# Performance work log

Measured on AMD Instinct MI355X. Metric: run time of the kernel, lower is better.

The kernel has to match this reference:

```python
import jax, jax.numpy as jnp
import numpy as np

WS = 8          # window_size
HEADS = 6
DH = 32         # dim_head


def _dwconv(t, w):
    # t: (B,C,H,W), w: (C,1,3,3) depthwise, stride 1, padding 1 -> SAME
    return jax.lax.conv_general_dilated(
        t, w, window_strides=(1, 1), padding='SAME',
        feature_group_count=t.shape[1],
        dimension_numbers=('NCHW', 'OIHW', 'NCHW'))


def _l2norm(t, eps=1e-12):
    # matches F.normalize: x / max(||x||, eps)
    n = jnp.sqrt(jnp.sum(t * t, axis=-1, keepdims=True))
    return t / jnp.maximum(n, eps)


def setup_inputs() -> dict:
    key = jax.random.key(0)
    ks = jax.random.split(key, 10)
    B, H, W, C = 2, 256, 256, 192
    s = 0.05
    return {
        'x': jax.random.normal(ks[0], (B, H, W, C), jnp.float32),
        'illu_fea_trans': jax.random.normal(ks[1], (B, H, W, C), jnp.float32),
        'gt_w': jax.random.normal(ks[2], (C, C), jnp.float32) * s,
        'gt_b': jax.random.normal(ks[3], (C,), jnp.float32) * s,
        'qkv_w': jax.random.normal(ks[4], (C, 3 * C), jnp.float32) * s,
        'qkv_b': jax.random.normal(ks[5], (3 * C,), jnp.float32) * s,
        'proj_w': jax.random.normal(ks[6], (C, C), jnp.float32) * s,
        'proj_b': jax.random.normal(ks[7], (C,), jnp.float32) * s,
        'conv1_w': jax.random.normal(ks[8], (C, 1, 3, 3), jnp.float32) * s,
        'conv2_w': jax.random.normal(ks[9], (C, 1, 3, 3), jnp.float32) * s,
    }


def reference(x, illu_fea_trans, gt_w, gt_b, qkv_w, qkv_b, proj_w, proj_b,
              conv1_w, conv2_w):
    B, H, W, C = x.shape
    Ws, heads, d = WS, HEADS, DH
    scale = d ** (-0.5)
    pad_h = (Ws - H % Ws) % Ws
    pad_w = (Ws - W % Ws) % Ws
    xp = jnp.pad(x, ((0, 0), (0, pad_h), (0, pad_w), (0, 0)), mode='reflect')
    ip = jnp.pad(illu_fea_trans, ((0, 0), (0, pad_h), (0, pad_w), (0, 0)), mode='reflect')
    Hp, Wp = xp.shape[1], xp.shape[2]
    nW = (Hp // Ws) * (Wp // Ws)
    T = Ws * Ws

    def to_windows(t):
        t = t.reshape(B, Hp // Ws, Ws, Wp // Ws, Ws, C)
        return t.transpose(0, 1, 3, 2, 4, 5).reshape(B * nW, T, C)

    xw = to_windows(xp)                                  # (B*nW, T, C)
    qkv = (xw @ qkv_w + qkv_b).reshape(B * nW, T, 3, heads, d)
    qkv = qkv.transpose(2, 0, 3, 1, 4)                   # (3, Bn, h, T, d)
    q, k, v = qkv[0], qkv[1], qkv[2]
    q = _l2norm(q)
    k = _l2norm(k)

    illu = to_windows(ip).reshape(B * nW, T, heads, d).transpose(0, 2, 1, 3)
    v = v * (1.0 + jax.nn.sigmoid(illu))

    # global token: avg-pool over padded spatial dims, then linear
    gt = jnp.mean(xp, axis=(1, 2)) @ gt_w + gt_b          # (B, C)
    gt = gt.reshape(B, heads, 1, d)
    # faithful to torch expand(dim=2 -> nW).reshape(B*nW, heads, 1, d)
    gk = jnp.broadcast_to(gt, (B, heads, nW, d)).reshape(B * nW, heads, 1, d)
    k = jnp.concatenate([k, gk], axis=2)                  # (Bn, h, T+1, d)
    v = jnp.concatenate([v, gk], axis=2)

    # chunked softmax over keys == full softmax over key axis (chunks on q only)
    attn = jax.nn.softmax(jnp.einsum('bhqd,bhkd->bhqk', q, k) * scale, axis=-1)
    out = jnp.einsum('bhqk,bhkd->bhqd', attn, v)          # (Bn, h, T, d)
    out = out.transpose(0, 2, 1, 3).reshape(B * nW, T, C)
    out = out @ proj_w + proj_b

    out = out.reshape(B, Hp // Ws, Wp // Ws, Ws, Ws, C)
    out = out.transpose(0, 1, 3, 2, 4, 5).reshape(B, Hp, Wp, C)[:, :H, :W, :]

    # depthwise-conv positional branch on padded x (exact gelu like torch)
    t = xp.transpose(0, 3, 1, 2)                          # (B,C,Hp,Wp)
    t = _dwconv(t, conv1_w)
    t = jax.nn.gelu(t, approximate=False)
    t = _dwconv(t, conv2_w)
    pos = t.transpose(0, 2, 3, 1)[:, :H, :W, :]
    return out + pos
```

## Files before the change

kernel.cpp:

```cpp
#include <hip/hip_runtime.h>
#include <hip/hip_bf16.h>

#define BB   2
#define HH   256
#define WWD  256
#define CC   192
#define WSZ  8
#define TT   64
#define NHD  6
#define DHD  32
#define N3   576

typedef __attribute__((ext_vector_type(8))) short short8;
typedef __attribute__((ext_vector_type(4))) float f32x4;

__device__ inline short bf16_bits(float f) {
  __hip_bfloat16 h = __float2bfloat16(f);
  return __builtin_bit_cast(short, h);
}

__device__ inline void stage1k(const short* gsrc, short* ldst, int lane) {
  __builtin_amdgcn_global_load_lds(
      (const __attribute__((address_space(1))) void*)(gsrc + lane * 8),
      (__attribute__((address_space(3))) void*)ldst, 16, 0, 0);
}

__global__ __launch_bounds__(256) void lcam_wshuf(const float* __restrict__ src,
                                                  short* __restrict__ dst,
                                                  int ncols, int nfrag, int perm) {
  int gid = blockIdx.x * 256 + threadIdx.x;
  if (gid >= nfrag) return;
  int lane = gid & 63;
  int s = (gid >> 6) % 6;
  int ct = gid / 384;
  int col = ct * 16 + (lane & 15);
  int k0 = s * 32 + (lane >> 4) * 8;
  short8 v;
#pragma unroll
  for (int j = 0; j < 8; ++j)
    v[j] = bf16_bits(src[(size_t)(k0 + j) * ncols + col]);
  int didx = perm ? ((s * (ncols / 16) + ct) * 64 + lane) : gid;
  *(short8*)(dst + (size_t)didx * 8) = v;
}

__global__ __launch_bounds__(256) void lcam_sum_x(const float* __restrict__ x,
                                                  float* __restrict__ sums) {
  int blk = blockIdx.x;
  int b = blk >> 9;
  int chunk = blk & 511;
  const float* xp = x + ((size_t)b * 65536 + (size_t)chunk * 128) * CC;
  int t = threadIdx.x;
  if (t < CC) {
    float acc = 0.f;
    for (int p = 0; p < 128; ++p) acc += xp[(size_t)p * CC + t];
    atomicAdd(&sums[b * CC + t], acc);
  }
}

__global__ void lcam_gt(const float* __restrict__ sums,
                        const float* __restrict__ gt_w,
                        const float* __restrict__ gt_b,
                        float* __restrict__ gt) {
  int b = blockIdx.x;
  int co = threadIdx.x;
  float acc = gt_b[co];
  const float inv = 1.f / 65536.f;
  for (int c = 0; c < CC; ++c)
    acc += sums[b * CC + c] * inv * gt_w[c * CC + co];
  gt[b * CC + co] = acc;
}

__global__ __launch_bounds__(256) void lcam_attn(
    const float* __restrict__ x, const float* __restrict__ illu,
    const short* __restrict__ wf, const short* __restrict__ pwf,
    const float* __restrict__ qkv_b, const float* __restrict__ proj_b,
    const float* __restrict__ gt, float* __restrict__ out) {
  __shared__ __align__(16) short wgt[2][6144];
  __shared__ __align__(16) short ks[65 * 40];
  __shared__ __align__(16) short vt[32 * 72];
  __shared__ __align__(16) short qs[64 * 40];
  __shared__ __align__(16) short ps[64 * 72];

  int w = blockIdx.x;
  int b  = w >> 10;
  int wy = (w >> 5) & 31;
  int wx = w & 31;
  int t  = threadIdx.x;
  int lane = t & 63;
  int rtile = t >> 6;
  int m = lane & 15;
  int quad = lane >> 4;
  int key0 = rtile * 16 + quad * 4;

  size_t base = ((size_t)(b * HH + wy * WSZ) * WWD + wx * WSZ) * CC;

#pragma unroll
  for (int u = 0; u < 3; ++u) {
    int ii = rtile * 3 + u;
    stage1k(wf + ii * 512, wgt[0] + ii * 512, lane);
  }

  int apix = rtile * 16 + m;
  size_t arow = base + (size_t)((apix >> 3) * WWD + (apix & 7)) * CC + quad * 8;
  short8 afrag[6];
#pragma unroll
  for (int s = 0; s < 6; ++s) {
    const float* ap = x + arow + s * 32;
    float4 f0 = *(const float4*)(ap);
    float4 f1 = *(const float4*)(ap + 4);
    short8 v;
    v[0] = bf16_bits(f0.x); v[1] = bf16_bits(f0.y);
    v[2] = bf16_bits(f0.z); v[3] = bf16_bits(f0.w);
    v[4] = bf16_bits(f1.x); v[5] = bf16_bits(f1.y);
    v[6] = bf16_bits(f1.z); v[7] = bf16_bits(f1.w);
    afrag[s] = v;
  }
  const short8* wA8 = (const short8*)wgt[0];
  const short8* wB8 = (const short8*)wgt[1];

  f32x4 pacc[12];
#pragma unroll
  for (int ct = 0; ct < 12; ++ct) {
    f32x4 z = {0.f, 0.f, 0.f, 0.f};
    pacc[ct] = z;
  }

  __syncthreads();

  for (int h = 0; h < NHD; ++h) {
#pragma unroll
    for (int u = 0; u < 3; ++u) {
      int ii = rtile * 3 + u;
      stage1k(wf + (12 + 2 * h) * 3072 + ii * 512, wgt[1] + ii * 512, lane);
    }
    float gv0 = gt[b * CC + h * 32 + m];
    float gv1 = gt[b * CC + h * 32 + 16 + m];
    float il0[4], il1[4];
#pragma unroll
    for (int r = 0; r < 4; ++r) {
      int key = key0 + r;
      const float* ip = illu + base + (size_t)((key >> 3) * WWD + (key & 7)) * CC + h * 32;
      il0[r] = ip[m];
      il1[r] = ip[16 + m];
    }
    {
      f32x4 a0 = {0.f,0.f,0.f,0.f}, a1 = {0.f,0.f,0.f,0.f};
      __builtin_amdgcn_s_setprio(1);
#pragma unroll
      for (int s = 0; s < 6; ++s)
        a0 = __builtin_amdgcn_mfma_f32_16x16x32_bf16(afrag[s], wA8[s*64 + lane], a0, 0,0,0);
#pragma unroll
      for (int s = 0; s < 6; ++s)
        a1 = __builtin_amdgcn_mfma_f32_16x16x32_bf16(afrag[s], wA8[384 + s*64 + lane], a1, 0,0,0);
      __builtin_amdgcn_s_setprio(0);
      float b0 = qkv_b[h*32 + m], b1 = qkv_b[h*32 + 16 + m];
#pragma unroll
      for (int r = 0; r < 4; ++r) {
        float v0 = a0[r] + b0, v1 = a1[r] + b1;
        float ss = v0*v0 + v1*v1;
        ss += __shfl_xor(ss, 1); ss += __shfl_xor(ss, 2);
        ss += __shfl_xor(ss, 4); ss += __shfl_xor(ss, 8);
        float scl = 0.17677669529663688f * __builtin_amdgcn_rsqf(fmaxf(ss, 1e-24f));
        int row = key0 + r;
        qs[row*40 + m]      = bf16_bits(v0 * scl);
        qs[row*40 + 16 + m] = bf16_bits(v1 * scl);
      }
    }
    __syncthreads();
#pragma unroll
    for (int u = 0; u < 3; ++u) {
      int ii = rtile * 3 + u;
      stage1k(wf + (24 + 2 * h) * 3072 + ii * 512, wgt[0] + ii * 512, lane);
    }
    {
      f32x4 a0 = {0.f,0.f,0.f,0.f}, a1 = {0.f,0.f,0.f,0.f};
      __builtin_amdgcn_s_setprio(1);
#pragma unroll
      for (int s = 0; s < 6; ++s)
        a0 = __builtin_amdgcn_mfma_f32_16x16x32_bf16(afrag[s], wB8[s*64 + lane], a0, 0,0,0);
#pragma unroll
      for (int s = 0; s < 6; ++s)
        a1 = __builtin_amdgcn_mfma_f32_16x16x32_bf16(afrag[s], wB8[384 + s*64 + lane], a1, 0,0,0);
      __builtin_amdgcn_s_setprio(0);
      float b0 = qkv_b[192 + h*32 + m], b1 = qkv_b[192 + h*32 + 16 + m];
#pragma unroll
      for (int r = 0; r < 4; ++r) {
        float v0 = a0[r] + b0, v1 = a1[r] + b1;
        float ss = v0*v0 + v1*v1;
        ss += __shfl_xor(ss, 1); ss += __shfl_xor(ss, 2);
        ss += __shfl_xor(ss, 4); ss += __shfl_xor(ss, 8);
        float scl = __builtin_amdgcn_rsqf(fmaxf(ss, 1e-24f));
        int row = key0 + r;
        ks[row*40 + m]      = bf16_bits(v0 * scl);
        ks[row*40 + 16 + m] = bf16_bits(v1 * scl);
      }
    }
    __syncthreads();
#pragma unroll
    for (int u = 0; u < 3; ++u) {
      int ii = rtile * 3 + u;
      stage1k(pwf + h * 6144 + ii * 512, wgt[1] + ii * 512, lane);
    }
    {
      f32x4 a0 = {0.f,0.f,0.f,0.f}, a1 = {0.f,0.f,0.f,0.f};
      __builtin_amdgcn_s_setprio(1);
#pragma unroll
      for (int s = 0; s < 6; ++s)
        a0 = __builtin_amdgcn_mfma_f32_16x16x32_bf16(afrag[s], wA8[s*64 + lane], a0, 0,0,0);
#pragma unroll
      for (int s = 0; s < 6; ++s)
        a1 = __builtin_amdgcn_mfma_f32_16x16x32_bf16(afrag[s], wA8[384 + s*64 + lane], a1, 0,0,0);
      __builtin_amdgcn_s_setprio(0);
      float b0 = qkv_b[384 + h*32 + m], b1 = qkv_b[384 + h*32 + 16 + m];
#pragma unroll
      for (int r = 0; r < 4; ++r) {
        int key = key0 + r;
        float s0 = __builtin_amdgcn_rcpf(1.f + __expf(-il0[r]));
        float s1 = __builtin_amdgcn_rcpf(1.f + __expf(-il1[r]));
        vt[m*72 + key]        = bf16_bits((a0[r] + b0) * (1.f + s0));
        vt[(16 + m)*72 + key] = bf16_bits((a1[r] + b1) * (1.f + s1));
      }
    }
    if (t < DHD) ks[64*40 + t] = bf16_bits(gt[b*CC + h*DHD + t]);
    __syncthreads();
    if (h < NHD - 1) {
#pragma unroll
      for (int u = 0; u < 3; ++u) {
        int ii = rtile * 3 + u;
        stage1k(wf + 2 * (h + 1) * 3072 + ii * 512, wgt[0] + ii * 512, lane);
      }
    }
    short8 qa = *(const short8*)(qs + (rtile*16 + m)*40 + quad*8);
    f32x4 sc[5];
#pragma unroll
    for (int ct = 0; ct < 4; ++ct) {
      short8 kb = *(const short8*)(ks + (ct*16 + m)*40 + quad*8);
      f32x4 z = {0.f,0.f,0.f,0.f};
      sc[ct] = __builtin_amdgcn_mfma_f32_16x16x32_bf16(qa, kb, z, 0,0,0);
    }
    {
      short8 kb = *(const short8*)(ks + 64*40 + quad*8);
      f32x4 z = {0.f,0.f,0.f,0.f};
      sc[4] = __builtin_amdgcn_mfma_f32_16x16x32_bf16(qa, kb, z, 0,0,0);
    }
    float p64v[4], invr[4];
#pragma unroll
    for (int r = 0; r < 4; ++r) {
      float e0 = __expf(sc[0][r]), e1 = __expf(sc[1][r]);
      float e2 = __expf(sc[2][r]), e3 = __expf(sc[3][r]);
      float e4 = (m == 0) ? __expf(sc[4][r]) : 0.f;
      int row = key0 + r;
      ps[row*72 + m]      = bf16_bits(e0);
      ps[row*72 + 16 + m] = bf16_bits(e1);
      ps[row*72 + 32 + m] = bf16_bits(e2);
      ps[row*72 + 48 + m] = bf16_bits(e3);
      float sum = e0 + e1 + e2 + e3 + e4;
      sum += __shfl_xor(sum, 1); sum += __shfl_xor(sum, 2);
      sum += __shfl_xor(sum, 4); sum += __shfl_xor(sum, 8);
      invr[r] = __builtin_amdgcn_rcpf(sum);
      p64v[r] = e4;
    }
    f32x4 o0 = {0.f,0.f,0.f,0.f}, o1 = {0.f,0.f,0.f,0.f};
    __builtin_amdgcn_s_setprio(1);
#pragma unroll
    for (int kc = 0; kc < 2; ++kc) {
      short8 pa  = *(const short8*)(ps + (rtile*16 + m)*72 + kc*32 + quad*8);
      short8 vb0 = *(const short8*)(vt + m*72        + kc*32 + quad*8);
      short8 vb1 = *(const short8*)(vt + (16 + m)*72 + kc*32 + quad*8);
      o0 = __builtin_amdgcn_mfma_f32_16x16x32_bf16(pa, vb0, o0, 0,0,0);
      o1 = __builtin_amdgcn_mfma_f32_16x16x32_bf16(pa, vb1, o1, 0,0,0);
    }
    __builtin_amdgcn_s_setprio(0);
#pragma unroll
    for (int r = 0; r < 4; ++r) {
      float pr = __shfl(p64v[r], lane & 48);
      int row = key0 + r;
      qs[row*40 + m]      = bf16_bits((o0[r] + pr * gv0) * invr[r]);
      qs[row*40 + 16 + m] = bf16_bits((o1[r] + pr * gv1) * invr[r]);
    }
    short8 oa = *(const short8*)(qs + (rtile*16 + m)*40 + quad*8);
    __builtin_amdgcn_s_setprio(1);
#pragma unroll
    for (int ct = 0; ct < 12; ++ct)
      pacc[ct] = __builtin_amdgcn_mfma_f32_16x16x32_bf16(oa, wB8[ct*64 + lane], pacc[ct], 0,0,0);
    __builtin_amdgcn_s_setprio(0);
    __syncthreads();
  }
#pragma unroll
  for (int ct = 0; ct < 12; ++ct) {
    float bias = proj_b[ct*16 + m];
#pragma unroll
    for (int r = 0; r < 4; ++r) {
      int row = key0 + r;
      out[base + (size_t)((row >> 3) * WWD + (row & 7)) * CC + ct*16 + m] = pacc[ct][r] + bias;
    }
  }
}

__global__ __launch_bounds__(256) void lcam_pos(const float* __restrict__ x,
                                                const float* __restrict__ w1,
                                                const float* __restrict__ w2,
                                                float* __restrict__ out) {
  __shared__ __align__(16) float xt[20 * 20 * 16];
  __shared__ float t1[18 * 18 * 16];
  __shared__ float wl1[16 * 9], wl2[16 * 9];
  int blk = blockIdx.x;
  int cgI = blk % 12; int tmp = blk / 12;
  int tx = tmp % 16; tmp /= 16;
  int ty = tmp % 16; int b = tmp / 16;
  int c0 = cgI * 16;
  int y0 = ty * 16, x0 = tx * 16;
  int t = threadIdx.x;
  if (t < 144) { wl1[t] = w1[c0 * 9 + t]; wl2[t] = w2[c0 * 9 + t]; }
  for (int vi = t; vi < 1600; vi += 256) {
    int cc4 = vi & 3;
    int lin = vi >> 2;
    int xx = lin % 20, yy = lin / 20;
    int gy = y0 - 2 + yy, gx = x0 - 2 + xx;
    float4 v = {0.f, 0.f, 0.f, 0.f};
    if (gy >= 0 && gy < HH && gx >= 0 && gx < WWD)
      v = *(const float4*)(x + (((size_t)b * HH + gy) * WWD + gx) * CC + c0 + cc4 * 4);
    *(float4*)(xt + (yy * 20 + xx) * 16 + cc4 * 4) = v;
  }
  __syncthreads();
  for (int idx = t; idx < 5184; idx += 256) {
    int cc = idx & 15;
    int xx = (idx >> 4) % 18;
    int yy = idx / 288;
    int gy = y0 - 1 + yy, gx = x0 - 1 + xx;
    float r = 0.f;
    if (gy >= 0 && gy < HH && gx >= 0 && gx < WWD) {
#pragma unroll
      for (int ky = 0; ky < 3; ++ky)
#pragma unroll
        for (int kx = 0; kx < 3; ++kx)
          r += xt[((yy + ky) * 20 + xx + kx) * 16 + cc] * wl1[cc * 9 + ky * 3 + kx];
      r = 0.5f * r * (1.f + erff(r * 0.70710678118654752f));
    }
    t1[(yy * 18 + xx) * 16 + cc] = r;
  }
  __syncthreads();
  for (int idx = t; idx < 4096; idx += 256) {
    int cc = idx & 15;
    int xx = (idx >> 4) & 15;
    int yy = idx >> 8;
    float r = 0.f;
#pragma unroll
    for (int ky = 0; ky < 3; ++ky)
#pragma unroll
      for (int kx = 0; kx < 3; ++kx)
        r += t1[((yy + ky) * 18 + xx + kx) * 16 + cc] * wl2[cc * 9 + ky * 3 + kx];
    size_t o = (((size_t)b * HH + y0 + yy) * WWD + x0 + xx) * CC + c0 + cc;
    out[o] += r;
  }
}

extern "C" void kernel_launch(void* const* d_in, const int* in_sizes, int n_in,
                              void* d_out, int out_size, void* d_ws, size_t ws_size,
                              hipStream_t stream) {
  const float* x       = (const float*)d_in[0];
  const float* illu    = (const float*)d_in[1];
  const float* gt_w    = (const float*)d_in[2];
  const float* gt_b    = (const float*)d_in[3];
  const float* qkv_w   = (const float*)d_in[4];
  const float* qkv_b   = (const float*)d_in[5];
  const float* proj_w  = (const float*)d_in[6];
  const float* proj_b  = (const float*)d_in[7];
  const float* conv1_w = (const float*)d_in[8];
  const float* conv2_w = (const float*)d_in[9];
  float* out = (float*)d_out;

  short* wf   = (short*)d_ws;
  short* pwf  = (short*)((char*)d_ws + 221184);
  float* sums = (float*)((char*)d_ws + 221184 + 73728);
  float* gt   = sums + BB * CC;

  hipMemsetAsync(sums, 0, BB * CC * sizeof(float), stream);
  lcam_wshuf<<<54, 256, 0, stream>>>(qkv_w, wf, N3, 36 * 6 * 64, 0);
  lcam_wshuf<<<18, 256, 0, stream>>>(proj_w, pwf, CC, 12 * 6 * 64, 1);
  lcam_sum_x<<<1024, 256, 0, stream>>>(x, sums);
  lcam_gt<<<BB, CC, 0, stream>>>(sums, gt_w, gt_b, gt);
  lcam_attn<<<2048, 256, 0, stream>>>(x, illu, wf, pwf, qkv_b, proj_b, gt, out);
  lcam_pos<<<6144, 256, 0, stream>>>(x, conv1_w, conv2_w, out);
}
```

Before: 504.4 us.

## Vectorize depthwise conv and channel sum, merge weight shuffle launches

The positional conv kernel now has each thread handle four channels with float4 LDS reads, keeps the 3x3 weights in registers, and does a float4 read-modify-write on the output. The channel-sum kernel reads float4 across four row groups and reduces them in shared memory before the atomics. The two weight-shuffle launches are merged into one kernel. The aim is fewer LDS and global instructions, better load parallelism in the reductions, and less launch overhead, at the cost of more registers in the conv kernel.

```diff
diff --git a/kernel.cpp b/kernel.cpp
--- a/kernel.cpp
+++ b/kernel.cpp
@@ -25,35 +25,54 @@
       (__attribute__((address_space(3))) void*)ldst, 16, 0, 0);
 }
 
-__global__ __launch_bounds__(256) void lcam_wshuf(const float* __restrict__ src,
-                                                  short* __restrict__ dst,
-                                                  int ncols, int nfrag, int perm) {
+__global__ __launch_bounds__(256) void lcam_wshuf2(const float* __restrict__ qkv_w,
+                                                   const float* __restrict__ proj_w,
+                                                   short* __restrict__ wf,
+                                                   short* __restrict__ pwf) {
   int gid = blockIdx.x * 256 + threadIdx.x;
-  if (gid >= nfrag) return;
-  int lane = gid & 63;
-  int s = (gid >> 6) % 6;
-  int ct = gid / 384;
+  const float* src; short* dst; int ncols, perm, g;
+  if (gid < 13824) { src = qkv_w; dst = wf; ncols = N3; perm = 0; g = gid; }
+  else {
+    g = gid - 13824;
+    if (g >= 4608) return;
+    src = proj_w; dst = pwf; ncols = CC; perm = 1;
+  }
+  int lane = g & 63;
+  int s = (g >> 6) % 6;
+  int ct = g / 384;
   int col = ct * 16 + (lane & 15);
   int k0 = s * 32 + (lane >> 4) * 8;
   short8 v;
 #pragma unroll
   for (int j = 0; j < 8; ++j)
     v[j] = bf16_bits(src[(size_t)(k0 + j) * ncols + col]);
-  int didx = perm ? ((s * (ncols / 16) + ct) * 64 + lane) : gid;
+  int didx = perm ? ((s * (ncols / 16) + ct) * 64 + lane) : g;
   *(short8*)(dst + (size_t)didx * 8) = v;
 }
 
-__global__ __launch_bounds__(256) void lcam_sum_x(const float* __restrict__ x,
+__global__ __launch_bounds__(192) void lcam_sum_x(const float* __restrict__ x,
                                                   float* __restrict__ sums) {
   int blk = blockIdx.x;
   int b = blk >> 9;
   int chunk = blk & 511;
-  const float* xp = x + ((size_t)b * 65536 + (size_t)chunk * 128) * CC;
+  const float4* xp = (const float4*)(x + ((size_t)b * 65536 + (size_t)chunk * 128) * CC);
   int t = threadIdx.x;
-  if (t < CC) {
-    float acc = 0.f;
-    for (int p = 0; p < 128; ++p) acc += xp[(size_t)p * CC + t];
-    atomicAdd(&sums[b * CC + t], acc);
+  int pg = t / 48, c4 = t % 48;
+  float4 acc = {0.f, 0.f, 0.f, 0.f};
+  for (int p = 0; p < 32; ++p) {
+    float4 v = xp[(size_t)(pg * 32 + p) * 48 + c4];
+    acc.x += v.x; acc.y += v.y; acc.z += v.z; acc.w += v.w;
+  }
+  __shared__ __align__(16) float4 red[192];
+  red[t] = acc;
+  __syncthreads();
+  if (pg == 0) {
+    float4 a0 = red[c4], a1 = red[48 + c4], a2 = red[96 + c4], a3 = red[144 + c4];
+    float* s = &sums[b * CC + c4 * 4];
+    atomicAdd(s + 0, a0.x + a1.x + a2.x + a3.x);
+    atomicAdd(s + 1, a0.y + a1.y + a2.y + a3.y);
+    atomicAdd(s + 2, a0.z + a1.z + a2.z + a3.z);
+    atomicAdd(s + 3, a0.w + a1.w + a2.w + a3.w);
   }
 }
 
@@ -302,7 +321,7 @@
                                                 const float* __restrict__ w2,
                                                 float* __restrict__ out) {
   __shared__ __align__(16) float xt[20 * 20 * 16];
-  __shared__ float t1[18 * 18 * 16];
+  __shared__ __align__(16) float t1[18 * 18 * 16];
   __shared__ float wl1[16 * 9], wl2[16 * 9];
   int blk = blockIdx.x;
   int cgI = blk % 12; int tmp = blk / 12;
@@ -311,47 +330,71 @@
   int c0 = cgI * 16;
   int y0 = ty * 16, x0 = tx * 16;
   int t = threadIdx.x;
+  int cc4 = t & 3;
   if (t < 144) { wl1[t] = w1[c0 * 9 + t]; wl2[t] = w2[c0 * 9 + t]; }
   for (int vi = t; vi < 1600; vi += 256) {
-    int cc4 = vi & 3;
+    int q4 = vi & 3;
     int lin = vi >> 2;
     int xx = lin % 20, yy = lin / 20;
     int gy = y0 - 2 + yy, gx = x0 - 2 + xx;
     float4 v = {0.f, 0.f, 0.f, 0.f};
     if (gy >= 0 && gy < HH && gx >= 0 && gx < WWD)
-      v = *(const float4*)(x + (((size_t)b * HH + gy) * WWD + gx) * CC + c0 + cc4 * 4);
-    *(float4*)(xt + (yy * 20 + xx) * 16 + cc4 * 4) = v;
+      v = *(const float4*)(x + (((size_t)b * HH + gy) * WWD + gx) * CC + c0 + q4 * 4);
+    *(float4*)(xt + (yy * 20 + xx) * 16 + q4 * 4) = v;
   }
   __syncthreads();
-  for (int idx = t; idx < 5184; idx += 256) {
-    int cc = idx & 15;
-    int xx = (idx >> 4) % 18;
-    int yy = idx / 288;
+  float w1r[4][9], w2r[4][9];
+#pragma unroll
+  for (int j = 0; j < 4; ++j)
+#pragma unroll
+    for (int k = 0; k < 9; ++k) {
+      w1r[j][k] = wl1[(cc4 * 4 + j) * 9 + k];
+      w2r[j][k] = wl2[(cc4 * 4 + j) * 9 + k];
+    }
+  for (int idx = t; idx < 1296; idx += 256) {
+    int lin = idx >> 2;
+    int xx = lin % 18, yy = lin / 18;
     int gy = y0 - 1 + yy, gx = x0 - 1 + xx;
-    float r = 0.f;
+    float4 r = {0.f, 0.f, 0.f, 0.f};
     if (gy >= 0 && gy < HH && gx >= 0 && gx < WWD) {
 #pragma unroll
       for (int ky = 0; ky < 3; ++ky)
 #pragma unroll
-        for (int kx = 0; kx < 3; ++kx)
-          r += xt[((yy + ky) * 20 + xx + kx) * 16 + cc] * wl1[cc * 9 + ky * 3 + kx];
-      r = 0.5f * r * (1.f + erff(r * 0.70710678118654752f));
-    }
-    t1[(yy * 18 + xx) * 16 + cc] = r;
+        for (int kx = 0; kx < 3; ++kx) {
+          float4 v = *(const float4*)(xt + ((yy + ky) * 20 + xx + kx) * 16 + cc4 * 4);
+          int k = ky * 3 + kx;
+          r.x += v.x * w1r[0][k];
+          r.y += v.y * w1r[1][k];
+          r.z += v.z * w1r[2][k];
+          r.w += v.w * w1r[3][k];
+        }
+      r.x = 0.5f * r.x * (1.f + erff(r.x * 0.70710678118654752f));
+      r.y = 0.5f * r.y * (1.f + erff(r.y * 0.70710678118654752f));
+      r.z = 0.5f * r.z * (1.f + erff(r.z * 0.70710678118654752f));
+      r.w = 0.5f * r.w * (1.f + erff(r.w * 0.70710678118654752f));
+    }
+    *(float4*)(t1 + (yy * 18 + xx) * 16 + cc4 * 4) = r;
   }
   __syncthreads();
-  for (int idx = t; idx < 4096; idx += 256) {
-    int cc = idx & 15;
-    int xx = (idx >> 4) & 15;
-    int yy = idx >> 8;
-    float r = 0.f;
+  for (int idx = t; idx < 1024; idx += 256) {
+    int lin = idx >> 2;
+    int xx = lin & 15, yy = lin >> 4;
+    float4 r = {0.f, 0.f, 0.f, 0.f};
 #pragma unroll
     for (int ky = 0; ky < 3; ++ky)
 #pragma unroll
-      for (int kx = 0; kx < 3; ++kx)
-        r += t1[((yy + ky) * 18 + xx + kx) * 16 + cc] * wl2[cc * 9 + ky * 3 + kx];
-    size_t o = (((size_t)b * HH + y0 + yy) * WWD + x0 + xx) * CC + c0 + cc;
-    out[o] += r;
+      for (int kx = 0; kx < 3; ++kx) {
+        float4 v = *(const float4*)(t1 + ((yy + ky) * 18 + xx + kx) * 16 + cc4 * 4);
+        int k = ky * 3 + kx;
+        r.x += v.x * w2r[0][k];
+        r.y += v.y * w2r[1][k];
+        r.z += v.z * w2r[2][k];
+        r.w += v.w * w2r[3][k];
+      }
+    size_t o = (((size_t)b * HH + y0 + yy) * WWD + x0 + xx) * CC + c0 + cc4 * 4;
+    float4 cur = *(float4*)(out + o);
+    cur.x += r.x; cur.y += r.y; cur.z += r.z; cur.w += r.w;
+    *(float4*)(out + o) = cur;
   }
 }
 
@@ -376,9 +419,8 @@
   float* gt   = sums + BB * CC;
 
   hipMemsetAsync(sums, 0, BB * CC * sizeof(float), stream);
-  lcam_wshuf<<<54, 256, 0, stream>>>(qkv_w, wf, N3, 36 * 6 * 64, 0);
-  lcam_wshuf<<<18, 256, 0, stream>>>(proj_w, pwf, CC, 12 * 6 * 64, 1);
-  lcam_sum_x<<<1024, 256, 0, stream>>>(x, sums);
+  lcam_wshuf2<<<72, 256, 0, stream>>>(qkv_w, proj_w, wf, pwf);
+  lcam_sum_x<<<1024, 192, 0, stream>>>(x, sums);
   lcam_gt<<<BB, CC, 0, stream>>>(sums, gt_w, gt_b, gt);
   lcam_attn<<<2048, 256, 0, stream>>>(x, illu, wf, pwf, qkv_b, proj_b, gt, out);
   lcam_pos<<<6144, 256, 0, stream>>>(x, conv1_w, conv2_w, out);
```

After: 532.6 us. +5.6%, slower.
